# Optimization experiments

Hardware: AMD Instinct MI355X
Metric: run time of the kernel (lower is better)

## Reference

```python
import jax, jax.numpy as jnp
import numpy as np

B, N, CIN, C, D, FH, FW = 4, 6, 256, 64, 41, 16, 44
OGW, OGH = 704, 256
NX0, NX1, NZ = 200, 200, 1
DX = np.array([0.5, 0.5, 20.0], np.float32)   # gen_dx_bx: step of each bound
BX = np.array([-49.75, -49.75, 0.0], np.float32)  # lower + dx/2


def _frustum():
    ds = np.broadcast_to(np.arange(4.0, 45.0, 1.0)[:, None, None], (D, FH, FW))
    xs = np.broadcast_to(np.linspace(0.0, OGW - 1.0, FW)[None, None, :], (D, FH, FW))
    ys = np.broadcast_to(np.linspace(0.0, OGH - 1.0, FH)[None, :, None], (D, FH, FW))
    return jnp.asarray(np.stack([xs, ys, ds], -1), jnp.float32)  # (D,FH,FW,3)


def _conv(x, w, b, p):
    y = jax.lax.conv_general_dilated(x, w, (1, 1), [(p, p), (p, p)],
                                     dimension_numbers=('NCHW', 'OIHW', 'NCHW'))
    return y + b[None, :, None, None]


def setup_inputs():
    key = jax.random.key(0)
    ks = jax.random.split(key, 16)
    feat = jax.random.normal(ks[0], (B * N, CIN, FH, FW), jnp.float32)
    # realistic calibration: 6 cameras yawed around ego, cam->ego axis swap
    Mcam = np.array([[0., 0., 1.], [-1., 0., 0.], [0., -1., 0.]], np.float32)
    rots = np.zeros((B, N, 3, 3), np.float32)
    for n in range(N):
        a = 2.0 * np.pi * n / N
        c, s = np.cos(a), np.sin(a)
        Rz = np.array([[c, -s, 0.], [s, c, 0.], [0., 0., 1.]], np.float32)
        rots[:, n] = Rz @ Mcam
    trans = np.zeros((B, N, 3), np.float32); trans[..., 2] = 1.5
    K = np.array([[350., 0., OGW / 2.], [0., 350., OGH / 2.], [0., 0., 1.]], np.float32)
    intrins = np.broadcast_to(K, (B, N, 3, 3)).copy()
    eye = np.broadcast_to(np.eye(3, dtype=np.float32), (B, N, 3, 3)).copy()
    warps = eye.copy(); post_rots = eye.copy()
    post_trans = np.zeros((B, N, 3), np.float32)
    def w_(k, o, i, kh, kw):
        return jax.random.normal(k, (o, i, kh, kw), jnp.float32) * np.float32(np.sqrt(2.0 / (i * kh * kw)))
    z = lambda o: jnp.zeros((o,), jnp.float32)
    params = dict(
        cam_w1=w_(ks[1], 256, CIN, 3, 3), cam_b1=z(256),
        cam_w2=w_(ks[2], 256, 256, 3, 3), cam_b2=z(256),
        cam_wl=w_(ks[3], C, 256, 1, 1), cam_bl=z(C),
        dep_w1=w_(ks[4], 256, CIN, 1, 1), dep_b1=z(256),
        dep_wl=w_(ks[5], D, 256, 1, 1), dep_bl=z(D),
        fus_w=jax.random.normal(ks[6], (C, C, 1, 1), jnp.float32) * 0.01,
        fus_b=jnp.full((C,), -4.595, jnp.float32),  # normal_init(std=0.01, bias=-4.595)
        bev_w1=w_(ks[7], 128, C, 3, 3), bev_b1=z(128),
        bev_w2=w_(ks[8], 128, 128, 3, 3), bev_b2=z(128),
        bev_wl=w_(ks[9], C, 128, 1, 1), bev_bl=z(C),
    )
    return dict(feat=feat, rots=jnp.asarray(rots), trans=jnp.asarray(trans),
                intrins=jnp.asarray(intrins), warps=jnp.asarray(warps),
                post_trans=jnp.asarray(post_trans), post_rots=jnp.asarray(post_rots), **params)


def reference(feat, rots, trans, intrins, warps, post_trans, post_rots,
              cam_w1, cam_b1, cam_w2, cam_b2, cam_wl, cam_bl,
              dep_w1, dep_b1, dep_wl, dep_bl,
              fus_w, fus_b, bev_w1, bev_b1, bev_w2, bev_b2, bev_wl, bev_bl):
    h = jax.nn.relu(_conv(feat, cam_w1, cam_b1, 1))
    h = jax.nn.relu(_conv(h, cam_w2, cam_b2, 1))
    img = _conv(h, cam_wl, cam_bl, 0)                              # (B*N, C, FH, FW)
    # --- depth encoder (stacked_convs=1, kernel 1x1) + softmax over depth bins ---
    d = jax.nn.relu(_conv(feat, dep_w1, dep_b1, 0))
    depth = jax.nn.softmax(_conv(d, dep_wl, dep_bl, 0), axis=1)    # (B*N, D, FH, FW)
    # --- lift: outer product of depth dist and image features ---
    ctx = depth[:, None] * img[:, :, None]                         # (B*N, C, D, FH, FW)
    ctx = ctx.reshape(B, N, C, D, FH, FW).transpose(0, 1, 3, 4, 5, 2)  # (B,N,D,FH,FW,C)
    # --- geometry: pixel frustum -> ego frame (post_rots/post_trans branch) ---
    fr = _frustum()
    pts = fr[None, None] - post_trans[:, :, None, None, None, :]
    pts = jnp.einsum('bnij,bndhwj->bndhwi', jnp.linalg.inv(post_rots), pts)
    pts = jnp.concatenate([pts[..., :2] * pts[..., 2:3], pts[..., 2:3]], -1)
    combine = rots @ jnp.linalg.inv(intrins)
    pts = jnp.einsum('bnij,bndhwj->bndhwi', combine, pts) + trans[:, :, None, None, None, :]
    # --- splat: voxel pooling via segment-sum (== LSS sort + cumsum trick) ---
    dx = jnp.asarray(DX); bx = jnp.asarray(BX)
    geom = ((pts - (bx - dx / 2.0)) / dx).astype(jnp.int32).reshape(-1, 3)
    bix = jnp.repeat(jnp.arange(B, dtype=jnp.int32), N * D * FH * FW)
    kept = ((geom[:, 0] >= 0) & (geom[:, 0] < NX0) &
            (geom[:, 1] >= 0) & (geom[:, 1] < NX1) &
            (geom[:, 2] >= 0) & (geom[:, 2] < NZ))
    nseg = NX0 * NX1 * NZ * B
    rank = geom[:, 0] * (NX1 * NZ * B) + geom[:, 1] * (NZ * B) + geom[:, 2] * B + bix
    rank = jnp.where(kept, rank, nseg)  # dropped points go to an overflow bucket
    pooled = jax.ops.segment_sum(ctx.reshape(-1, C), rank, num_segments=nseg + 1)[:-1]
    # bev_xy_transpose=True layout: (B, C, nz, nx0, nx1), then unbind z into channels
    bev = pooled.reshape(NX0, NX1, NZ, B, C).transpose(3, 4, 2, 0, 1).reshape(B, C * NZ, NX0, NX1)
    # --- multi-scale fusion + BEV encoder ---
    bev = _conv(bev, fus_w, fus_b, 0)
    h = jax.nn.relu(_conv(bev, bev_w1, bev_b1, 1))
    h = jax.nn.relu(_conv(h, bev_w2, bev_b2, 1))
    return _conv(h, bev_wl, bev_bl, 0)                             # (B, C, NX0, NX1)
```

## Files before the change

### kernel.cpp

```cpp
#include <hip/hip_runtime.h>
#include <hip/hip_bf16.h>

typedef unsigned short u16;
typedef __bf16 bf16x8 __attribute__((ext_vector_type(8)));
typedef float f32x4 __attribute__((ext_vector_type(4)));

#define NB 4
#define NCAM 6
#define NBN 24
#define CIN 256
#define CC 64
#define ND 41
#define FH 16
#define FW 44
#define NX 200
#define BPL ((size_t)NB * NX * NX * 32)

#define WS_FEATT_HI 0ul
#define WS_FEATT_LO 8650752ul
#define WS_H1_HI    17301504ul
#define WS_H2_HI    34603008ul
#define WS_H1D      51904512ul
#define WS_BW1_HI   69206016ul
#define WS_BW1_LO   69353472ul
#define WS_BEV0     76302336ul
#define WS_CW1_HI   117262336ul
#define WS_CW1_LO   118441984ul
#define WS_CW2_HI   119621632ul
#define WS_CW2_LO   120801280ul
#define WS_CWL_HI   121980928ul
#define WS_CWL_LO   122013696ul
#define WS_DW1_HI   122046464ul
#define WS_DW1_LO   122177536ul
#define WS_DEP      122308608ul
#define WS_IMGT     125079552ul
#define WS_MATS     129404928ul
#define WS_FUSW_HI  129406656ul
#define WS_FUSW_LO  129414848ul
#define WS_BEV1_HI  0ul
#define WS_HB1_HI   81920000ul
#define WS_HB2_HI   0ul
#define WS_BW2_HI   163840000ul
#define WS_BW2_LO   164134912ul
#define WS_BWL_HI   164429824ul
#define WS_BWL_LO   164446208ul

__device__ inline u16 f2bf_rne(float x) {
  unsigned u = __float_as_uint(x);
  unsigned r = u + 0x7fffu + ((u >> 16) & 1u);
  return (u16)(r >> 16);
}
__device__ inline float bf2f(u16 h) { return __uint_as_float(((unsigned)h) << 16); }
__device__ inline void split_bf(float x, u16& hi, u16& lo) {
  hi = f2bf_rne(x);
  lo = f2bf_rne(x - bf2f(hi));
}
__device__ inline f32x4 mfma16(bf16x8 a, bf16x8 b, f32x4 c) {
  return __builtin_amdgcn_mfma_f32_16x16x32_bf16(a, b, c, 0, 0, 0);
}
__device__ inline bf16x8 ld8(const u16* p) { return *(const bf16x8*)p; }

__global__ __launch_bounds__(256) void featsplit(const float* __restrict__ in,
    u16* __restrict__ oh, u16* __restrict__ ol) {
  int nh = blockIdx.x;
  int n = nh >> 4, h = nh & 15;
  __shared__ float lds[256][44];
  int tid = threadIdx.x;
  for (int e = tid; e < 256 * 44; e += 256) {
    int ci = e / 44, w = e % 44;
    lds[ci][w] = in[((n * CIN + ci) * FH + h) * FW + w];
  }
  __syncthreads();
  for (int e = tid; e < 256 * 44; e += 256) {
    int w = e / 256, ci = e % 256;
    u16 hi, lo;
    split_bf(lds[ci][w], hi, lo);
    size_t o = ((size_t)((n * FH + h) * FW + w)) * 256 + ci;
    oh[o] = hi; ol[o] = lo;
  }
}

__global__ __launch_bounds__(256) void wsplit3(const float* __restrict__ src,
    u16* __restrict__ dhi, u16* __restrict__ dlo, int CO, int CI_) {
  int idx = blockIdx.x * 256 + threadIdx.x;
  if (idx >= CO * CI_ * 9) return;
  int co = idx / (CI_ * 9);
  int r = idx % (CI_ * 9);
  int ci = r / 9, t = r % 9;
  u16 h, l;
  split_bf(src[idx], h, l);
  int o = (t * CO + co) * CI_ + ci;
  dhi[o] = h; dlo[o] = l;
}

__global__ __launch_bounds__(256) void wsplit1(const float* __restrict__ src,
    u16* __restrict__ dhi, u16* __restrict__ dlo, int n) {
  int i = blockIdx.x * 256 + threadIdx.x;
  if (i >= n) return;
  u16 h, l;
  split_bf(src[i], h, l);
  dhi[i] = h; dlo[i] = l;
}

__global__ void prep_mats(const float* __restrict__ rots, const float* __restrict__ intrins,
                          const float* __restrict__ post_rots, float* __restrict__ mats) {
  int bn = threadIdx.x;
  if (bn >= NBN) return;
  {
    const float* A = intrins + bn * 9;
    double a0=A[0],a1=A[1],a2=A[2],a3=A[3],a4=A[4],a5=A[5],a6=A[6],a7=A[7],a8=A[8];
    double det = a0*(a4*a8 - a5*a7) - a1*(a3*a8 - a5*a6) + a2*(a3*a7 - a4*a6);
    float inv[9];
    inv[0] = (float)((a4*a8 - a5*a7) / det);
    inv[1] = (float)((a2*a7 - a1*a8) / det);
    inv[2] = (float)((a1*a5 - a2*a4) / det);
    inv[3] = (float)((a5*a6 - a3*a8) / det);
    inv[4] = (float)((a0*a8 - a2*a6) / det);
    inv[5] = (float)((a2*a3 - a0*a5) / det);
    inv[6] = (float)((a3*a7 - a4*a6) / det);
    inv[7] = (float)((a1*a6 - a0*a7) / det);
    inv[8] = (float)((a0*a4 - a1*a3) / det);
    const float* R = rots + bn * 9;
    #pragma unroll
    for (int i = 0; i < 3; ++i)
      #pragma unroll
      for (int j = 0; j < 3; ++j) {
        float s = __fadd_rn(__fadd_rn(__fmul_rn(R[i*3+0], inv[0*3+j]),
                                      __fmul_rn(R[i*3+1], inv[1*3+j])),
                            __fmul_rn(R[i*3+2], inv[2*3+j]));
        mats[bn * 9 + i * 3 + j] = s;
      }
  }
  {
    const float* A = post_rots + bn * 9;
    double a0=A[0],a1=A[1],a2=A[2],a3=A[3],a4=A[4],a5=A[5],a6=A[6],a7=A[7],a8=A[8];
    double det = a0*(a4*a8 - a5*a7) - a1*(a3*a8 - a5*a6) + a2*(a3*a7 - a4*a6);
    float* o = mats + 216 + bn * 9;
    o[0] = (float)((a4*a8 - a5*a7) / det);
    o[1] = (float)((a2*a7 - a1*a8) / det);
    o[2] = (float)((a1*a5 - a2*a4) / det);
    o[3] = (float)((a5*a6 - a3*a8) / det);
    o[4] = (float)((a0*a8 - a2*a6) / det);
    o[5] = (float)((a2*a3 - a0*a5) / det);
    o[6] = (float)((a3*a7 - a4*a6) / det);
    o[7] = (float)((a1*a6 - a0*a7) / det);
    o[8] = (float)((a0*a4 - a1*a3) / det);
  }
}

__global__ __launch_bounds__(256, 2) void cam_mfma(
    const u16* __restrict__ Gh,
    const u16* __restrict__ Wh,
    const float* __restrict__ bias, u16* __restrict__ Oh) {
  int nh = blockIdx.x;
  int n = nh >> 4, h = nh & 15;
  __shared__ u16 Ah[3 * 50 * 44];
  __shared__ u16 Bh[2][256 * 44];
  int tid = threadIdx.x;
  int wv = tid >> 6, l = tid & 63;
  int l15 = l & 15, kq = l >> 4;
  f32x4 acc[3][4] = {};
  const uint4 z4 = {0u, 0u, 0u, 0u};
  for (int cc = 0; cc < 8; ++cc) {
    __syncthreads();
    for (int e = tid; e < 600; e += 256) {
      int q = e & 3;
      int c = (e >> 2) % 50;
      int r = e / 200;
      int hh = h + r - 1, ww = c - 1;
      int off = (r * 50 + c) * 44 + q * 8;
      uint4 vh = z4;
      if (hh >= 0 && hh < FH && ww >= 0 && ww < FW) {
        size_t g = ((size_t)((n * FH + hh) * FW + ww)) * 256 + cc * 32 + q * 8;
        vh = *(const uint4*)&Gh[g];
      }
      *(uint4*)&Ah[off] = vh;
    }
    for (int p = 0; p < 5; ++p) {
      int t0 = 2 * p;
      int nt = (t0 + 1 < 9) ? 2 : 1;
      __syncthreads();
      for (int e = tid; e < nt * 1024; e += 256) {
        int tp = e >> 10;
        int rem = e & 1023;
        int q = rem & 3, co = rem >> 2;
        size_t g = ((size_t)((t0 + tp) * 256 + co)) * 256 + cc * 32 + q * 8;
        *(uint4*)&Bh[tp][co * 44 + q * 8] = *(const uint4*)&Wh[g];
      }
      __syncthreads();
      for (int tp = 0; tp < nt; ++tp) {
        int t = t0 + tp;
        int ty = t / 3, tx = t % 3;
        bf16x8 bh[4];
        #pragma unroll
        for (int nf = 0; nf < 4; ++nf)
          bh[nf] = *(const bf16x8*)&Bh[tp][(wv * 64 + nf * 16 + l15) * 44 + kq * 8];
        #pragma unroll
        for (int mf = 0; mf < 3; ++mf) {
          int o = (ty * 50 + mf * 16 + l15 + tx) * 44 + kq * 8;
          bf16x8 ah = *(const bf16x8*)&Ah[o];
          #pragma unroll
          for (int nf = 0; nf < 4; ++nf)
            acc[mf][nf] = mfma16(ah, bh[nf], acc[mf][nf]);
        }
      }
    }
  }
  __syncthreads();
  #pragma unroll
  for (int mf = 0; mf < 3; ++mf)
    #pragma unroll
    for (int nf = 0; nf < 4; ++nf) {
      int co = wv * 64 + nf * 16 + l15;
      float bv = bias[co];
      #pragma unroll
      for (int r = 0; r < 4; ++r) {
        int x = mf * 16 + kq * 4 + r;
        if (x < FW)
          Bh[0][x * 256 + co] = f2bf_rne(fmaxf(acc[mf][nf][r] + bv, 0.f));
      }
    }
  __syncthreads();
  for (int uid = tid; uid < FW * 32; uid += 256) {
    int x = uid >> 5, c16 = uid & 31;
    *(uint4*)&Oh[(((size_t)((n * FH + h) * FW + x)) * 256) + c16 * 8] =
        *(const uint4*)&Bh[0][x * 256 + c16 * 8];
  }
}

template <int CI_>
__global__ __launch_bounds__(256, 3) void bev_mfma(
    const u16* __restrict__ Gh,
    const u16* __restrict__ Wh,
    const float* __restrict__ bias, u16* __restrict__ Oh) {
  int tile = blockIdx.x;
  int b = blockIdx.y;
  int y0 = (tile / 13) * 16, x0 = (tile % 13) * 16;
  __shared__ u16 Ah[18 * 18 * 32];
  __shared__ u16 Bh[2][128 * 44];
  int tid = threadIdx.x;
  int wv = tid >> 6, l = tid & 63;
  int l15 = l & 15, kq = l >> 4;
  f32x4 acc[4][8] = {};
  const uint4 z4 = {0u, 0u, 0u, 0u};
  for (int cc = 0; cc < CI_ / 32; ++cc) {
    __syncthreads();
    for (int e = tid; e < 1296; e += 256) {
      int q = e & 3;
      int dx = (e >> 2) % 18;
      int dy = e / 72;
      int gy = y0 + dy - 1, gx = x0 + dx - 1;
      int row = dy * 18 + dx;
      int off = row * 32 + ((q ^ ((row >> 1) & 3)) * 8);
      uint4 vh = z4;
      if (gy >= 0 && gy < NX && gx >= 0 && gx < NX) {
        size_t g = (size_t)cc * BPL + ((size_t)((b * NX + gy) * NX + gx)) * 32 + q * 8;
        vh = *(const uint4*)&Gh[g];
      }
      *(uint4*)&Ah[off] = vh;
    }
    for (int p = 0; p < 5; ++p) {
      int t0 = 2 * p;
      int nt = (t0 + 1 < 9) ? 2 : 1;
      __syncthreads();
      for (int e = tid; e < nt * 512; e += 256) {
        int tp = e >> 9;
        int rem = e & 511;
        int q = rem & 3, co = rem >> 2;
        size_t g = ((size_t)((t0 + tp) * 128 + co)) * CI_ + cc * 32 + q * 8;
        *(uint4*)&Bh[tp][co * 44 + q * 8] = *(const uint4*)&Wh[g];
      }
      __syncthreads();
      for (int tp = 0; tp < nt; ++tp) {
        int t = t0 + tp;
        int ty = t / 3, tx = t % 3;
        bf16x8 bh[8];
        #pragma unroll
        for (int nf = 0; nf < 8; ++nf)
          bh[nf] = *(const bf16x8*)&Bh[tp][(nf * 16 + l15) * 44 + kq * 8];
        #pragma unroll
        for (int mf = 0; mf < 4; ++mf) {
          int row = (wv * 4 + mf + ty) * 18 + (l15 + tx);
          int o = row * 32 + ((kq ^ ((row >> 1) & 3)) * 8);
          bf16x8 ah = *(const bf16x8*)&Ah[o];
          #pragma unroll
          for (int nf = 0; nf < 8; ++nf)
            acc[mf][nf] = mfma16(ah, bh[nf], acc[mf][nf]);
        }
      }
    }
  }
  u16* st = Ah;
  for (int mf = 0; mf < 4; ++mf) {
    __syncthreads();
    #pragma unroll
    for (int nf = 0; nf < 8; ++nf) {
      int co = nf * 16 + l15;
      float bv = bias[co];
      #pragma unroll
      for (int r = 0; r < 4; ++r) {
        int xx = kq * 4 + r;
        st[(wv * 16 + xx) * 128 + co] = f2bf_rne(fmaxf(acc[mf][nf][r] + bv, 0.f));
      }
    }
    __syncthreads();
    #pragma unroll
    for (int k = 0; k < 4; ++k) {
      int uid = tid + k * 256;
      int pos = uid >> 4, c16 = uid & 15;
      int wvp = pos >> 4, xx = pos & 15;
      int yy = y0 + wvp * 4 + mf, gx = x0 + xx;
      if (yy < NX && gx < NX) {
        int ch = c16 >> 2, qq = c16 & 3;
        *(uint4*)&Oh[(size_t)ch * BPL + ((size_t)((b * NX + yy) * NX + gx)) * 32 + qq * 8] =
            *(const uint4*)&st[pos * 128 + c16 * 8];
      }
    }
  }
}

__global__ __launch_bounds__(256) void lin_mfma(const u16* __restrict__ Gh,
    const u16* __restrict__ Wh,
    const float* __restrict__ bias, float* __restrict__ out) {
  int wv = threadIdx.x >> 6, l = threadIdx.x & 63;
  int l15 = l & 15, kq = l >> 4;
  int pos0 = blockIdx.x * 256 + wv * 64;
  f32x4 acc[4][4] = {};
  for (int ks = 0; ks < 8; ++ks) {
    bf16x8 bh[4], ah[4];
    #pragma unroll
    for (int nf = 0; nf < 4; ++nf)
      bh[nf] = ld8(Wh + (nf * 16 + l15) * 256 + ks * 32 + kq * 8);
    #pragma unroll
    for (int mf = 0; mf < 4; ++mf)
      ah[mf] = ld8(Gh + ((size_t)(pos0 + mf * 16 + l15)) * 256 + ks * 32 + kq * 8);
    #pragma unroll
    for (int mf = 0; mf < 4; ++mf)
      #pragma unroll
      for (int nf = 0; nf < 4; ++nf)
        acc[mf][nf] = mfma16(ah[mf], bh[nf], acc[mf][nf]);
  }
  #pragma unroll
  for (int mf = 0; mf < 4; ++mf)
    #pragma unroll
    for (int nf = 0; nf < 4; ++nf) {
      float bv = bias[nf * 16 + l15];
      #pragma unroll
      for (int r = 0; r < 4; ++r) {
        int pos = pos0 + mf * 16 + kq * 4 + r;
        out[(size_t)pos * 64 + nf * 16 + l15] = acc[mf][nf][r] + bv;
      }
    }
}

__global__ __launch_bounds__(256) void dep1_mfma(const u16* __restrict__ Gh,
    const u16* __restrict__ Gl, const u16* __restrict__ Wh, const u16* __restrict__ Wl,
    const float* __restrict__ bias, float* __restrict__ out) {
  int wv = threadIdx.x >> 6, l = threadIdx.x & 63;
  int l15 = l & 15, kq = l >> 4;
  int pos0 = blockIdx.x * 256 + wv * 64;
  int cog = blockIdx.y * 64;
  f32x4 acc[4][4] = {};
  for (int ks = 0; ks < 8; ++ks) {
    bf16x8 bh[4], bl[4], ah[4], al[4];
    #pragma unroll
    for (int nf = 0; nf < 4; ++nf) {
      int o = (cog + nf * 16 + l15) * 256 + ks * 32 + kq * 8;
      bh[nf] = ld8(Wh + o); bl[nf] = ld8(Wl + o);
    }
    #pragma unroll
    for (int mf = 0; mf < 4; ++mf) {
      size_t o = ((size_t)(pos0 + mf * 16 + l15)) * 256 + ks * 32 + kq * 8;
      ah[mf] = ld8(Gh + o); al[mf] = ld8(Gl + o);
    }
    #pragma unroll
    for (int mf = 0; mf < 4; ++mf)
      #pragma unroll
      for (int nf = 0; nf < 4; ++nf) {
        acc[mf][nf] = mfma16(ah[mf], bh[nf], acc[mf][nf]);
        acc[mf][nf] = mfma16(ah[mf], bl[nf], acc[mf][nf]);
        acc[mf][nf] = mfma16(al[mf], bh[nf], acc[mf][nf]);
      }
  }
  #pragma unroll
  for (int mf = 0; mf < 4; ++mf)
    #pragma unroll
    for (int nf = 0; nf < 4; ++nf) {
      int co = cog + nf * 16 + l15;
      float bv = bias[co];
      #pragma unroll
      for (int r = 0; r < 4; ++r) {
        int pos = pos0 + mf * 16 + kq * 4 + r;
        out[(size_t)pos * 256 + co] = fmaxf(acc[mf][nf][r] + bv, 0.f);
      }
    }
}

__global__ __launch_bounds__(256) void fus_mfma(const float* __restrict__ in,
    const u16* __restrict__ Wh, const u16* __restrict__ Wl,
    const float* __restrict__ bias, u16* __restrict__ oh) {
  int wv = threadIdx.x >> 6, l = threadIdx.x & 63;
  int l15 = l & 15, kq = l >> 4;
  int pos0 = blockIdx.x * 256 + wv * 64;
  f32x4 acc[4][4] = {};
  for (int ks = 0; ks < 2; ++ks) {
    bf16x8 bh[4], bl[4], ah[4], al[4];
    #pragma unroll
    for (int nf = 0; nf < 4; ++nf) {
      int o = (nf * 16 + l15) * 64 + ks * 32 + kq * 8;
      bh[nf] = ld8(Wh + o); bl[nf] = ld8(Wl + o);
    }
    #pragma unroll
    for (int mf = 0; mf < 4; ++mf) {
      size_t o = ((size_t)(pos0 + mf * 16 + l15)) * 64 + ks * 32 + kq * 8;
      float4 v0 = *(const float4*)&in[o];
      float4 v1 = *(const float4*)&in[o + 4];
      float xs[8] = {v0.x, v0.y, v0.z, v0.w, v1.x, v1.y, v1.z, v1.w};
      u16 th[8], tl[8];
      #pragma unroll
      for (int i = 0; i < 8; ++i) split_bf(xs[i], th[i], tl[i]);
      ah[mf] = *(const bf16x8*)th;
      al[mf] = *(const bf16x8*)tl;
    }
    #pragma unroll
    for (int mf = 0; mf < 4; ++mf)
      #pragma unroll
      for (int nf = 0; nf < 4; ++nf) {
        acc[mf][nf] = mfma16(ah[mf], bh[nf], acc[mf][nf]);
        acc[mf][nf] = mfma16(ah[mf], bl[nf], acc[mf][nf]);
        acc[mf][nf] = mfma16(al[mf], bh[nf], acc[mf][nf]);
      }
  }
  #pragma unroll
  for (int mf = 0; mf < 4; ++mf)
    #pragma unroll
    for (int nf = 0; nf < 4; ++nf) {
      int c = nf * 16 + l15;
      int ch = c >> 5, cw = c & 31;
      float bv = bias[c];
      #pragma unroll
      for (int r = 0; r < 4; ++r) {
        int pos = pos0 + mf * 16 + kq * 4 + r;
        oh[(size_t)ch * BPL + (size_t)pos * 32 + cw] = f2bf_rne(acc[mf][nf][r] + bv);
      }
    }
}

__global__ __launch_bounds__(256) void out_mfma(const u16* __restrict__ Wh,
    const u16* __restrict__ Wl, const u16* __restrict__ Gh,
    const float* __restrict__ bias, float* __restrict__ out) {
  int wv = threadIdx.x >> 6, l = threadIdx.x & 63;
  int l15 = l & 15, kq = l >> 4;
  int pos0 = blockIdx.x * 256 + wv * 64;
  f32x4 acc[4][4] = {};
  for (int ks = 0; ks < 4; ++ks) {
    bf16x8 ah[4], al[4], bh[4];
    #pragma unroll
    for (int mf = 0; mf < 4; ++mf) {
      int o = (mf * 16 + l15) * 128 + ks * 32 + kq * 8;
      ah[mf] = ld8(Wh + o); al[mf] = ld8(Wl + o);
    }
    #pragma unroll
    for (int nf = 0; nf < 4; ++nf)
      bh[nf] = ld8(Gh + (size_t)ks * BPL + ((size_t)(pos0 + nf * 16 + l15)) * 32 + kq * 8);
    #pragma unroll
    for (int mf = 0; mf < 4; ++mf)
      #pragma unroll
      for (int nf = 0; nf < 4; ++nf) {
        acc[mf][nf] = mfma16(ah[mf], bh[nf], acc[mf][nf]);
        acc[mf][nf] = mfma16(al[mf], bh[nf], acc[mf][nf]);
      }
  }
  #pragma unroll
  for (int mf = 0; mf < 4; ++mf)
    #pragma unroll
    for (int r = 0; r < 4; ++r) {
      int co = mf * 16 + kq * 4 + r;
      float bv = bias[co];
      #pragma unroll
      for (int nf = 0; nf < 4; ++nf) {
        int pos = pos0 + nf * 16 + l15;
        int b = pos / 40000;
        int xy = pos - b * 40000;
        out[((size_t)(b * CC + co)) * 40000 + xy] = acc[mf][nf][r] + bv;
      }
    }
}

__global__ __launch_bounds__(256) void dep_softmax(const float* __restrict__ in,
    const float* __restrict__ wt, const float* __restrict__ bias, float* __restrict__ depth) {
  int nh = blockIdx.x;
  int n = nh >> 4, h = nh & 15;
  __shared__ float lds[256][49];
  __shared__ float lg[ND][FW];
  int tid = threadIdx.x;
  for (int e = tid; e < 256 * 48; e += 256) {
    int ci = e % 256, w = e / 256;
    lds[ci][w] = (w < FW) ? in[((size_t)((n * FH + h) * FW + w)) * 256 + ci] : 0.f;
  }
  __syncthreads();
  int co = tid >> 2, wseg = tid & 3;
  int ob = wseg * 12;
  int nj = (wseg == 3) ? 8 : 12;
  if (co < ND) {
    float acc[12];
    #pragma unroll
    for (int j = 0; j < 12; ++j) acc[j] = 0.f;
    const float* wp = wt + co * 256;
    for (int ci = 0; ci < 256; ++ci) {
      float wv = wp[ci];
      #pragma unroll
      for (int j = 0; j < 12; ++j) acc[j] += wv * lds[ci][ob + j];
    }
    float b = bias[co];
    for (int j = 0; j < nj; ++j) lg[co][ob + j] = acc[j] + b;
  }
  __syncthreads();
  if (tid < FW) {
    int w = tid;
    float m = lg[0][w];
    #pragma unroll
    for (int d = 1; d < ND; ++d) m = fmaxf(m, lg[d][w]);
    float s = 0.f;
    #pragma unroll
    for (int d = 0; d < ND; ++d) s += expf(lg[d][w] - m);
    #pragma unroll
    for (int d = 0; d < ND; ++d)
      depth[((n * ND + d) * FH + h) * FW + w] = expf(lg[d][w] - m) / s;
  }
}

__global__ __launch_bounds__(256) void splat(const float* __restrict__ depth,
    const float* __restrict__ img, const float* __restrict__ mats,
    const float* __restrict__ trans, const float* __restrict__ ptrans,
    float* __restrict__ bev0) {
  int gid = blockIdx.x * 4 + (threadIdx.x >> 6);
  int c = threadIdx.x & 63;
  int w = gid % FW;
  int t = gid / FW;
  int d = t % ND;
  int bn = t / ND;
  int b = bn / NCAM;
  float fx = (w == FW - 1) ? 703.0f : (float)((double)w * (703.0 / 43.0));
  float fz = (float)(4 + d);
  const float* pt = ptrans + bn * 3;
  const float* P = mats + 216 + bn * 9;
  const float* M = mats + bn * 9;
  const float* tr = trans + bn * 3;
  float px = __fsub_rn(fx, pt[0]);
  float pz = __fsub_rn(fz, pt[2]);
  const float* dp = depth + ((size_t)(bn * ND + d) * FH) * FW + w;
  const float* ip = img + ((size_t)(bn * FH) * FW + w) * CC + c;
  int cell = -1;
  float acc = 0.f;
  for (int h = 0; h < FH; ++h) {
    float fy = (float)(17 * h);
    float py = __fsub_rn(fy, pt[1]);
    float q0 = __fadd_rn(__fadd_rn(__fmul_rn(P[0], px), __fmul_rn(P[1], py)), __fmul_rn(P[2], pz));
    float q1 = __fadd_rn(__fadd_rn(__fmul_rn(P[3], px), __fmul_rn(P[4], py)), __fmul_rn(P[5], pz));
    float q2 = __fadd_rn(__fadd_rn(__fmul_rn(P[6], px), __fmul_rn(P[7], py)), __fmul_rn(P[8], pz));
    float r0 = __fmul_rn(q0, q2), r1 = __fmul_rn(q1, q2), r2 = q2;
    float u0 = __fadd_rn(__fadd_rn(__fadd_rn(__fmul_rn(M[0], r0), __fmul_rn(M[1], r1)), __fmul_rn(M[2], r2)), tr[0]);
    float u1 = __fadd_rn(__fadd_rn(__fadd_rn(__fmul_rn(M[3], r0), __fmul_rn(M[4], r1)), __fmul_rn(M[5], r2)), tr[1]);
    float u2 = __fadd_rn(__fadd_rn(__fadd_rn(__fmul_rn(M[6], r0), __fmul_rn(M[7], r1)), __fmul_rn(M[8], r2)), tr[2]);
    int gx = (int)__fmul_rn(__fadd_rn(u0, 50.0f), 2.0f);
    int gy = (int)__fmul_rn(__fadd_rn(u1, 50.0f), 2.0f);
    int gz = (int)__fdiv_rn(__fadd_rn(u2, 10.0f), 20.0f);
    bool kept = (gx >= 0 && gx < NX && gy >= 0 && gy < NX && gz == 0);
    int c2 = kept ? (b * NX + gx) * NX + gy : -1;
    if (c2 != cell) {
      if (cell >= 0) atomicAdd(&bev0[(size_t)cell * CC + c], acc);
      cell = c2;
      acc = 0.f;
    }
    if (kept)
      acc = __fadd_rn(acc, __fmul_rn(dp[h * FW], ip[(size_t)h * FW * CC]));
  }
  if (cell >= 0) atomicAdd(&bev0[(size_t)cell * CC + c], acc);
}

extern "C" void kernel_launch(void* const* d_in, const int* in_sizes, int n_in,
                              void* d_out, int out_size, void* d_ws, size_t ws_size,
                              hipStream_t stream) {
  const float* feat       = (const float*)d_in[0];
  const float* rots       = (const float*)d_in[1];
  const float* trans      = (const float*)d_in[2];
  const float* intrins    = (const float*)d_in[3];
  const float* post_trans = (const float*)d_in[5];
  const float* post_rots  = (const float*)d_in[6];
  const float* cam_w1 = (const float*)d_in[7];
  const float* cam_b1 = (const float*)d_in[8];
  const float* cam_w2 = (const float*)d_in[9];
  const float* cam_b2 = (const float*)d_in[10];
  const float* cam_wl = (const float*)d_in[11];
  const float* cam_bl = (const float*)d_in[12];
  const float* dep_w1 = (const float*)d_in[13];
  const float* dep_b1 = (const float*)d_in[14];
  const float* dep_wl = (const float*)d_in[15];
  const float* dep_bl = (const float*)d_in[16];
  const float* fus_w  = (const float*)d_in[17];
  const float* fus_b  = (const float*)d_in[18];
  const float* bev_w1 = (const float*)d_in[19];
  const float* bev_b1 = (const float*)d_in[20];
  const float* bev_w2 = (const float*)d_in[21];
  const float* bev_b2 = (const float*)d_in[22];
  const float* bev_wl = (const float*)d_in[23];
  const float* bev_bl = (const float*)d_in[24];

  char* wsb = (char*)d_ws;
  u16* featT_h = (u16*)(wsb + WS_FEATT_HI);
  u16* featT_l = (u16*)(wsb + WS_FEATT_LO);
  u16* h1_h = (u16*)(wsb + WS_H1_HI);
  u16* h2_h = (u16*)(wsb + WS_H2_HI);
  float* h1d = (float*)(wsb + WS_H1D);
  u16* bw1_h = (u16*)(wsb + WS_BW1_HI);
  u16* bw1_l = (u16*)(wsb + WS_BW1_LO);
  float* bev0 = (float*)(wsb + WS_BEV0);
  u16* cw1_h = (u16*)(wsb + WS_CW1_HI);
  u16* cw1_l = (u16*)(wsb + WS_CW1_LO);
  u16* cw2_h = (u16*)(wsb + WS_CW2_HI);
  u16* cw2_l = (u16*)(wsb + WS_CW2_LO);
  u16* cwl_h = (u16*)(wsb + WS_CWL_HI);
  u16* cwl_l = (u16*)(wsb + WS_CWL_LO);
  u16* dw1_h = (u16*)(wsb + WS_DW1_HI);
  u16* dw1_l = (u16*)(wsb + WS_DW1_LO);
  float* dep  = (float*)(wsb + WS_DEP);
  float* imgt = (float*)(wsb + WS_IMGT);
  float* mats = (float*)(wsb + WS_MATS);
  u16* fusw_h = (u16*)(wsb + WS_FUSW_HI);
  u16* fusw_l = (u16*)(wsb + WS_FUSW_LO);
  u16* bev1_h = (u16*)(wsb + WS_BEV1_HI);
  u16* hb1_h = (u16*)(wsb + WS_HB1_HI);
  u16* hb2_h = (u16*)(wsb + WS_HB2_HI);
  u16* bw2_h = (u16*)(wsb + WS_BW2_HI);
  u16* bw2_l = (u16*)(wsb + WS_BW2_LO);
  u16* bwl_h = (u16*)(wsb + WS_BWL_HI);
  u16* bwl_l = (u16*)(wsb + WS_BWL_LO);

  featsplit<<<NBN * FH, 256, 0, stream>>>(feat, featT_h, featT_l);
  wsplit3<<<2304, 256, 0, stream>>>(cam_w1, cw1_h, cw1_l, 256, 256);
  wsplit3<<<2304, 256, 0, stream>>>(cam_w2, cw2_h, cw2_l, 256, 256);
  wsplit3<<<288, 256, 0, stream>>>(bev_w1, bw1_h, bw1_l, 128, 64);
  wsplit3<<<576, 256, 0, stream>>>(bev_w2, bw2_h, bw2_l, 128, 128);
  wsplit1<<<64, 256, 0, stream>>>(cam_wl, cwl_h, cwl_l, 64 * 256);
  wsplit1<<<256, 256, 0, stream>>>(dep_w1, dw1_h, dw1_l, 256 * 256);
  wsplit1<<<32, 256, 0, stream>>>(bev_wl, bwl_h, bwl_l, 64 * 128);
  wsplit1<<<16, 256, 0, stream>>>(fus_w, fusw_h, fusw_l, 64 * 64);
  prep_mats<<<1, 32, 0, stream>>>(rots, intrins, post_rots, mats);

  cam_mfma<<<NBN * FH, 256, 0, stream>>>(featT_h, cw1_h, cam_b1, h1_h);
  cam_mfma<<<NBN * FH, 256, 0, stream>>>(h1_h, cw2_h, cam_b2, h2_h);
  lin_mfma<<<66, 256, 0, stream>>>(h2_h, cwl_h, cam_bl, imgt);

  dep1_mfma<<<dim3(66, 4), 256, 0, stream>>>(featT_h, featT_l, dw1_h, dw1_l, dep_b1, h1d);
  dep_softmax<<<NBN * FH, 256, 0, stream>>>(h1d, dep_wl, dep_bl, dep);

  hipMemsetAsync((void*)bev0, 0, 40960000ul, stream);
  splat<<<(NBN * ND * FW) / 4, 256, 0, stream>>>(dep, imgt, mats, trans, post_trans, bev0);

  fus_mfma<<<625, 256, 0, stream>>>(bev0, fusw_h, fusw_l, fus_b, bev1_h);
  bev_mfma<64><<<dim3(169, NB), 256, 0, stream>>>(bev1_h, bw1_h, bev_b1, hb1_h);
  bev_mfma<128><<<dim3(169, NB), 256, 0, stream>>>(hb1_h, bw2_h, bev_b2, hb2_h);
  out_mfma<<<625, 256, 0, stream>>>(bwl_h, bwl_l, hb2_h, bev_bl, (float*)d_out);
}
```

Measured before the change: 531.7 us.

## Split output channels across grid dimension in cam and BEV conv kernels

The cam and BEV 3x3 conv kernels now split output channels into two halves along a new grid dimension. This doubles the block count, halves each block's accumulators and weight tile, and raises the occupancy hint from 2 or 3 to 4 blocks. It targets underfilled grids: 384 blocks for cam and 676 for BEV on a GPU with many compute units. The cost is that every input halo tile is loaded twice. The BEV epilogue staging also gains an XOR-style swizzle to reduce LDS bank conflicts.

```diff
diff --git a/kernel.cpp b/kernel.cpp
--- a/kernel.cpp
+++ b/kernel.cpp
@@ -148,18 +148,19 @@
   }
 }
 
-__global__ __launch_bounds__(256, 2) void cam_mfma(
+__global__ __launch_bounds__(256, 4) void cam_mfma(
     const u16* __restrict__ Gh,
     const u16* __restrict__ Wh,
     const float* __restrict__ bias, u16* __restrict__ Oh) {
   int nh = blockIdx.x;
   int n = nh >> 4, h = nh & 15;
+  int cog = blockIdx.y * 128;
   __shared__ u16 Ah[3 * 50 * 44];
-  __shared__ u16 Bh[2][256 * 44];
+  __shared__ u16 Bh[2][128 * 44];
   int tid = threadIdx.x;
   int wv = tid >> 6, l = tid & 63;
   int l15 = l & 15, kq = l >> 4;
-  f32x4 acc[3][4] = {};
+  f32x4 acc[3][2] = {};
   const uint4 z4 = {0u, 0u, 0u, 0u};
   for (int cc = 0; cc < 8; ++cc) {
     __syncthreads();
@@ -180,27 +181,27 @@
       int t0 = 2 * p;
       int nt = (t0 + 1 < 9) ? 2 : 1;
       __syncthreads();
-      for (int e = tid; e < nt * 1024; e += 256) {
-        int tp = e >> 10;
-        int rem = e & 1023;
+      for (int e = tid; e < nt * 512; e += 256) {
+        int tp = e >> 9;
+        int rem = e & 511;
         int q = rem & 3, co = rem >> 2;
-        size_t g = ((size_t)((t0 + tp) * 256 + co)) * 256 + cc * 32 + q * 8;
+        size_t g = ((size_t)((t0 + tp) * 256 + cog + co)) * 256 + cc * 32 + q * 8;
         *(uint4*)&Bh[tp][co * 44 + q * 8] = *(const uint4*)&Wh[g];
       }
       __syncthreads();
       for (int tp = 0; tp < nt; ++tp) {
         int t = t0 + tp;
         int ty = t / 3, tx = t % 3;
-        bf16x8 bh[4];
+        bf16x8 bh[2];
         #pragma unroll
-        for (int nf = 0; nf < 4; ++nf)
-          bh[nf] = *(const bf16x8*)&Bh[tp][(wv * 64 + nf * 16 + l15) * 44 + kq * 8];
+        for (int nf = 0; nf < 2; ++nf)
+          bh[nf] = *(const bf16x8*)&Bh[tp][(wv * 32 + nf * 16 + l15) * 44 + kq * 8];
         #pragma unroll
         for (int mf = 0; mf < 3; ++mf) {
           int o = (ty * 50 + mf * 16 + l15 + tx) * 44 + kq * 8;
           bf16x8 ah = *(const bf16x8*)&Ah[o];
           #pragma unroll
-          for (int nf = 0; nf < 4; ++nf)
+          for (int nf = 0; nf < 2; ++nf)
             acc[mf][nf] = mfma16(ah, bh[nf], acc[mf][nf]);
         }
       }
@@ -210,38 +211,39 @@
   #pragma unroll
   for (int mf = 0; mf < 3; ++mf)
     #pragma unroll
-    for (int nf = 0; nf < 4; ++nf) {
-      int co = wv * 64 + nf * 16 + l15;
-      float bv = bias[co];
+    for (int nf = 0; nf < 2; ++nf) {
+      int col = wv * 32 + nf * 16 + l15;
+      float bv = bias[cog + col];
       #pragma unroll
       for (int r = 0; r < 4; ++r) {
         int x = mf * 16 + kq * 4 + r;
         if (x < FW)
-          Bh[0][x * 256 + co] = f2bf_rne(fmaxf(acc[mf][nf][r] + bv, 0.f));
+          Bh[0][x * 128 + col] = f2bf_rne(fmaxf(acc[mf][nf][r] + bv, 0.f));
       }
     }
   __syncthreads();
-  for (int uid = tid; uid < FW * 32; uid += 256) {
-    int x = uid >> 5, c16 = uid & 31;
-    *(uint4*)&Oh[(((size_t)((n * FH + h) * FW + x)) * 256) + c16 * 8] =
-        *(const uint4*)&Bh[0][x * 256 + c16 * 8];
+  for (int uid = tid; uid < FW * 16; uid += 256) {
+    int x = uid >> 4, c16 = uid & 15;
+    *(uint4*)&Oh[(((size_t)((n * FH + h) * FW + x)) * 256) + cog + c16 * 8] =
+        *(const uint4*)&Bh[0][x * 128 + c16 * 8];
   }
 }
 
 template <int CI_>
-__global__ __launch_bounds__(256, 3) void bev_mfma(
+__global__ __launch_bounds__(256, 4) void bev_mfma(
     const u16* __restrict__ Gh,
     const u16* __restrict__ Wh,
     const float* __restrict__ bias, u16* __restrict__ Oh) {
   int tile = blockIdx.x;
   int b = blockIdx.y;
+  int cog = blockIdx.z * 64;
   int y0 = (tile / 13) * 16, x0 = (tile % 13) * 16;
   __shared__ u16 Ah[18 * 18 * 32];
-  __shared__ u16 Bh[2][128 * 44];
+  __shared__ u16 Bh[2][64 * 44];
   int tid = threadIdx.x;
   int wv = tid >> 6, l = tid & 63;
   int l15 = l & 15, kq = l >> 4;
-  f32x4 acc[4][8] = {};
+  f32x4 acc[4][4] = {};
   const uint4 z4 = {0u, 0u, 0u, 0u};
   for (int cc = 0; cc < CI_ / 32; ++cc) {
     __syncthreads();
@@ -263,20 +265,20 @@
       int t0 = 2 * p;
       int nt = (t0 + 1 < 9) ? 2 : 1;
       __syncthreads();
-      for (int e = tid; e < nt * 512; e += 256) {
-        int tp = e >> 9;
-        int rem = e & 511;
+      for (int e = tid; e < nt * 256; e += 256) {
+        int tp = e >> 8;
+        int rem = e & 255;
         int q = rem & 3, co = rem >> 2;
-        size_t g = ((size_t)((t0 + tp) * 128 + co)) * CI_ + cc * 32 + q * 8;
+        size_t g = ((size_t)((t0 + tp) * 128 + cog + co)) * CI_ + cc * 32 + q * 8;
         *(uint4*)&Bh[tp][co * 44 + q * 8] = *(const uint4*)&Wh[g];
       }
       __syncthreads();
       for (int tp = 0; tp < nt; ++tp) {
         int t = t0 + tp;
         int ty = t / 3, tx = t % 3;
-        bf16x8 bh[8];
+        bf16x8 bh[4];
         #pragma unroll
-        for (int nf = 0; nf < 8; ++nf)
+        for (int nf = 0; nf < 4; ++nf)
           bh[nf] = *(const bf16x8*)&Bh[tp][(nf * 16 + l15) * 44 + kq * 8];
         #pragma unroll
         for (int mf = 0; mf < 4; ++mf) {
@@ -284,7 +286,7 @@
           int o = row * 32 + ((kq ^ ((row >> 1) & 3)) * 8);
           bf16x8 ah = *(const bf16x8*)&Ah[o];
           #pragma unroll
-          for (int nf = 0; nf < 8; ++nf)
+          for (int nf = 0; nf < 4; ++nf)
             acc[mf][nf] = mfma16(ah, bh[nf], acc[mf][nf]);
         }
       }
@@ -294,26 +296,29 @@
   for (int mf = 0; mf < 4; ++mf) {
     __syncthreads();
     #pragma unroll
-    for (int nf = 0; nf < 8; ++nf) {
+    for (int nf = 0; nf < 4; ++nf) {
       int co = nf * 16 + l15;
-      float bv = bias[co];
+      int cw = co >> 3;
+      float bv = bias[cog + co];
       #pragma unroll
       for (int r = 0; r < 4; ++r) {
         int xx = kq * 4 + r;
-        st[(wv * 16 + xx) * 128 + co] = f2bf_rne(fmaxf(acc[mf][nf][r] + bv, 0.f));
+        int row = wv * 16 + xx;
+        st[row * 64 + (((cw + row) & 7) * 8) + (co & 7)] =
+            f2bf_rne(fmaxf(acc[mf][nf][r] + bv, 0.f));
       }
     }
     __syncthreads();
     #pragma unroll
-    for (int k = 0; k < 4; ++k) {
+    for (int k = 0; k < 2; ++k) {
       int uid = tid + k * 256;
-      int pos = uid >> 4, c16 = uid & 15;
+      int pos = uid >> 3, c16 = uid & 7;
       int wvp = pos >> 4, xx = pos & 15;
       int yy = y0 + wvp * 4 + mf, gx = x0 + xx;
       if (yy < NX && gx < NX) {
-        int ch = c16 >> 2, qq = c16 & 3;
-        *(uint4*)&Oh[(size_t)ch * BPL + ((size_t)((b * NX + yy) * NX + gx)) * 32 + qq * 8] =
-            *(const uint4*)&st[pos * 128 + c16 * 8];
+        int chg = (cog >> 5) + (c16 >> 2), qq = c16 & 3;
+        *(uint4*)&Oh[(size_t)chg * BPL + ((size_t)((b * NX + yy) * NX + gx)) * 32 + qq * 8] =
+            *(const uint4*)&st[pos * 64 + (((c16 + pos) & 7) * 8)];
       }
     }
   }
@@ -648,8 +653,8 @@
   wsplit1<<<16, 256, 0, stream>>>(fus_w, fusw_h, fusw_l, 64 * 64);
   prep_mats<<<1, 32, 0, stream>>>(rots, intrins, post_rots, mats);
 
-  cam_mfma<<<NBN * FH, 256, 0, stream>>>(featT_h, cw1_h, cam_b1, h1_h);
-  cam_mfma<<<NBN * FH, 256, 0, stream>>>(h1_h, cw2_h, cam_b2, h2_h);
+  cam_mfma<<<dim3(NBN * FH, 2), 256, 0, stream>>>(featT_h, cw1_h, cam_b1, h1_h);
+  cam_mfma<<<dim3(NBN * FH, 2), 256, 0, stream>>>(h1_h, cw2_h, cam_b2, h2_h);
   lin_mfma<<<66, 256, 0, stream>>>(h2_h, cwl_h, cam_bl, imgt);
 
   dep1_mfma<<<dim3(66, 4), 256, 0, stream>>>(featT_h, featT_l, dw1_h, dw1_l, dep_b1, h1d);
@@ -659,7 +664,7 @@
   splat<<<(NBN * ND * FW) / 4, 256, 0, stream>>>(dep, imgt, mats, trans, post_trans, bev0);
 
   fus_mfma<<<625, 256, 0, stream>>>(bev0, fusw_h, fusw_l, fus_b, bev1_h);
-  bev_mfma<64><<<dim3(169, NB), 256, 0, stream>>>(bev1_h, bw1_h, bev_b1, hb1_h);
-  bev_mfma<128><<<dim3(169, NB), 256, 0, stream>>>(hb1_h, bw2_h, bev_b2, hb2_h);
+  bev_mfma<64><<<dim3(169, NB, 2), 256, 0, stream>>>(bev1_h, bw1_h, bev_b1, hb1_h);
+  bev_mfma<128><<<dim3(169, NB, 2), 256, 0, stream>>>(hb1_h, bw2_h, bev_b2, hb2_h);
   out_mfma<<<625, 256, 0, stream>>>(bwl_h, bwl_l, hb2_h, bev_bl, (float*)d_out);
 }
```

Measured after the change: 451.4 us (median of 2 runs). 1.18x faster.
